# Kernel tuning notes

Hardware: AMD Instinct MI355X
Metric: run time of the kernel (lower is better)

Reference implementation:

```python
import jax, jax.numpy as jnp
import numpy as np

B, S, E, H, V, C = 1024, 64, 256, 512, 128, 32


def setup_inputs() -> dict:
    key = jax.random.key(0)
    ks = jax.random.split(key, 12)
    s = 0.05
    emb_table = jax.random.normal(ks[0], (V, E), jnp.float32) * s
    emb_table = emb_table.at[0].set(0.0)  # padding_idx = 0
    return {
        "x_in": jax.random.randint(ks[1], (B, S), 0, V),
        "x_lens": jax.random.randint(ks[2], (B,), 1, S + 1),
        "emb_table": emb_table,
        "W_ih": jax.random.normal(ks[3], (H, E), jnp.float32) * s,
        "b_ih": jnp.zeros((H,), jnp.float32),
        "W_hh": jax.random.normal(ks[4], (H, H), jnp.float32) * s,
        "b_hh": jnp.zeros((H,), jnp.float32),
        "W1": jax.random.normal(ks[5], (H, H), jnp.float32) * s,
        "b1": jnp.zeros((H,), jnp.float32),
        "W2": jax.random.normal(ks[6], (C, H), jnp.float32) * s,
        "b2": jnp.zeros((C,), jnp.float32),
    }


def reference(x_in, x_lens, emb_table, W_ih, b_ih, W_hh, b_hh, W1, b1, W2, b2):
    # Embedding lookup: [B, S, E]
    x_emb = emb_table[x_in]

    # Elman RNN: h_t = tanh(x_t W_ih^T + b_ih + h_{t-1} W_hh^T + b_hh)
    def step(h, x_t):
        h = jnp.tanh(x_t @ W_ih.T + b_ih + h @ W_hh.T + b_hh)
        return h, h

    h0 = jnp.zeros((x_in.shape[0], W_hh.shape[0]), x_emb.dtype)
    _, ys = jax.lax.scan(step, h0, jnp.swapaxes(x_emb, 0, 1))  # ys: [S, B, H]
    y_out = jnp.swapaxes(ys, 0, 1)  # [B, S, H]

    # column_gather: pick hidden state at position x_lens-1 for each row
    last = y_out[jnp.arange(y_out.shape[0]), x_lens - 1]  # [B, H]

    # MLP head (dropout is identity in eval mode)
    hidden = jax.nn.relu(last @ W1.T + b1)
    logits = hidden @ W2.T + b2  # [B, C]
    return logits
```

## Files before the change

kernel.cpp:

```cpp
#include <hip/hip_runtime.h>
#include <hip/hip_bf16.h>

#define BB 1024
#define SS 64
#define EE 256
#define HH 512
#define VV 128
#define CC 32

typedef _Float16 f16;
typedef _Float16 f16x4 __attribute__((ext_vector_type(4)));
typedef _Float16 f16x8 __attribute__((ext_vector_type(8)));
typedef float    f32x4 __attribute__((ext_vector_type(4)));

__global__ __launch_bounds__(256) void prep_P(
    const float* __restrict__ emb, const float* __restrict__ W_ih,
    const float* __restrict__ b_ih, const float* __restrict__ b_hh,
    f16* __restrict__ P)
{
    __shared__ float er[EE];
    const int v = blockIdx.x;
    for (int i = threadIdx.x; i < EE; i += 256) er[i] = emb[(size_t)v * EE + i];
    __syncthreads();
    for (int h = threadIdx.x; h < HH; h += 256) {
        const float4* wr = (const float4*)(W_ih + (size_t)h * EE);
        float s = 0.f;
        #pragma unroll 4
        for (int e4 = 0; e4 < EE / 4; ++e4) {
            float4 w = wr[e4];
            const float* e = er + e4 * 4;
            s += w.x * e[0] + w.y * e[1] + w.z * e[2] + w.w * e[3];
        }
        P[(size_t)v * HH + h] = (f16)(s + b_ih[h] + b_hh[h]);
    }
}

__global__ __launch_bounds__(256) void prep_W(
    const float* __restrict__ W_hh, f16* __restrict__ Wf)
{
    const int i = blockIdx.x * 256 + threadIdx.x;
    float4 x = ((const float4*)W_hh)[i];
    f16x4 y;
    y[0] = (f16)x.x; y[1] = (f16)x.y; y[2] = (f16)x.z; y[3] = (f16)x.w;
    *(f16x4*)(Wf + (size_t)i * 4) = y;
}

#define KSREG 12
#define KSLDS 4
#define HSTR  520

#define KB(t,k) "v"(bfr[t][k])
#define KBT(t)  KB(t,0), KB(t,1), KB(t,2), KB(t,3), KB(t,4), KB(t,5), \
                KB(t,6), KB(t,7), KB(t,8), KB(t,9), KB(t,10), KB(t,11)

__global__
__attribute__((amdgpu_flat_work_group_size(512, 512)))
__attribute__((amdgpu_waves_per_eu(2, 2)))
void rnn_kernel(
    const int* __restrict__ x_in, const int* __restrict__ x_lens,
    const f16* __restrict__ Wf, const f16* __restrict__ P,
    f16* __restrict__ last)
{
    __shared__ __align__(16) f16 hbuf[16 * HSTR];
    __shared__ __align__(16) f16 wlds[8 * 4 * KSLDS * 64 * 8];
    __shared__ int xin[16 * SS];
    __shared__ int lens[16];

    const int tid  = threadIdx.x;
    const int r0   = blockIdx.x * 16;
    const int wave = tid >> 6;
    const int lane = tid & 63;
    const int lrow = lane & 15;
    const int quad = lane >> 4;
    const int n0w  = wave * 64;

    f16x8 bfr[4][KSREG];
    #pragma unroll
    for (int t = 0; t < 4; ++t) {
        const f16* wr = Wf + (size_t)(n0w + 16 * t + lrow) * HH + quad * 8;
        #pragma unroll
        for (int ks = 0; ks < KSREG; ++ks)
            bfr[t][ks] = *(const f16x8*)(wr + ks * 32);
        #pragma unroll
        for (int ks = 0; ks < KSLDS; ++ks)
            *(f16x8*)(wlds + ((((wave * 4 + t) * KSLDS + ks) * 64 + lane) << 3)) =
                *(const f16x8*)(wr + (KSREG + ks) * 32);
    }

    for (int i = tid; i < 16 * (SS / 4); i += 512)
        ((int4*)xin)[i] = ((const int4*)(x_in + (size_t)r0 * SS))[i];
    if (tid < 16) lens[tid] = x_lens[r0 + tid];
    __syncthreads();

    const int   mylen = lens[lrow];
    const f16*  arow  = hbuf + lrow * HSTR + quad * 8;
    f16*        hwr   = hbuf + lrow * HSTR + n0w + quad * 4;
    f16*        lwr   = last + (size_t)(r0 + lrow) * HH + n0w + quad * 4;
    const f16*  pbase = P + n0w + quad * 4;

    for (int st = 0; st < SS; ++st) {
        asm volatile("" :: KBT(0), KBT(1), KBT(2), KBT(3));

        f32x4 acc0 = {0,0,0,0}, acc1 = {0,0,0,0}, acc2 = {0,0,0,0}, acc3 = {0,0,0,0};
        if (st) {
            #pragma unroll
            for (int ks = 0; ks < KSREG; ++ks) {
                f16x8 a = *(const f16x8*)(arow + ks * 32);
                acc0 = __builtin_amdgcn_mfma_f32_16x16x32_f16(bfr[0][ks], a, acc0, 0, 0, 0);
                acc1 = __builtin_amdgcn_mfma_f32_16x16x32_f16(bfr[1][ks], a, acc1, 0, 0, 0);
                acc2 = __builtin_amdgcn_mfma_f32_16x16x32_f16(bfr[2][ks], a, acc2, 0, 0, 0);
                acc3 = __builtin_amdgcn_mfma_f32_16x16x32_f16(bfr[3][ks], a, acc3, 0, 0, 0);
            }
            #pragma unroll
            for (int ks = 0; ks < KSLDS; ++ks) {
                f16x8 a  = *(const f16x8*)(arow + (KSREG + ks) * 32);
                f16x8 b0 = *(const f16x8*)(wlds + ((((wave * 4 + 0) * KSLDS + ks) * 64 + lane) << 3));
                f16x8 b1 = *(const f16x8*)(wlds + ((((wave * 4 + 1) * KSLDS + ks) * 64 + lane) << 3));
                f16x8 b2 = *(const f16x8*)(wlds + ((((wave * 4 + 2) * KSLDS + ks) * 64 + lane) << 3));
                f16x8 b3 = *(const f16x8*)(wlds + ((((wave * 4 + 3) * KSLDS + ks) * 64 + lane) << 3));
                acc0 = __builtin_amdgcn_mfma_f32_16x16x32_f16(b0, a, acc0, 0, 0, 0);
                acc1 = __builtin_amdgcn_mfma_f32_16x16x32_f16(b1, a, acc1, 0, 0, 0);
                acc2 = __builtin_amdgcn_mfma_f32_16x16x32_f16(b2, a, acc2, 0, 0, 0);
                acc3 = __builtin_amdgcn_mfma_f32_16x16x32_f16(b3, a, acc3, 0, 0, 0);
            }
        }

        const int  tok = xin[lrow * SS + st];
        const f16* pb  = pbase + (size_t)tok * HH;
        f16x4 pv0 = *(const f16x4*)(pb);
        f16x4 pv1 = *(const f16x4*)(pb + 16);
        f16x4 pv2 = *(const f16x4*)(pb + 32);
        f16x4 pv3 = *(const f16x4*)(pb + 48);

        __syncthreads();

        const int tp1 = st + 1;
        const bool wr_last = (mylen == tp1);
        #pragma unroll
        for (int t = 0; t < 4; ++t) {
            const f32x4 acc = (t == 0) ? acc0 : (t == 1) ? acc1 : (t == 2) ? acc2 : acc3;
            const f16x4 pv  = (t == 0) ? pv0  : (t == 1) ? pv1  : (t == 2) ? pv2  : pv3;
            f16x4 hv;
            #pragma unroll
            for (int r = 0; r < 4; ++r) {
                float z = acc[r] + (float)pv[r];
                float e = __expf(2.f * z);
                hv[r] = (f16)(1.f - 2.f / (e + 1.f));
            }
            *(f16x4*)(hwr + 16 * t) = hv;
            if (wr_last) *(f16x4*)(lwr + 16 * t) = hv;
        }

        __syncthreads();
    }
}

__global__ __launch_bounds__(256, 1)
void mlp1_kernel(
    const f16* __restrict__ last, const float* __restrict__ W1,
    const float* __restrict__ b1, f16* __restrict__ hidden)
{
    __shared__ __align__(16) f16 hb[16 * HSTR];
    const int tid   = threadIdx.x;
    const int g     = blockIdx.x & 63;
    const int slice = blockIdx.x >> 6;
    const int r0    = g * 16;
    const int n0    = slice * 64;
    const int wave  = tid >> 6;
    const int lane  = tid & 63;
    const int lrow  = lane & 15;
    const int quad  = lane >> 4;

    f16x8 bfr[16];
    {
        const float* wr = W1 + (size_t)(n0 + wave * 16 + lrow) * HH + quad * 8;
        #pragma unroll
        for (int K0 = 0; K0 < 16; ++K0) {
            float4 x0 = *(const float4*)(wr + K0 * 32);
            float4 x1 = *(const float4*)(wr + K0 * 32 + 4);
            f16x8 b;
            b[0] = (f16)x0.x; b[1] = (f16)x0.y; b[2] = (f16)x0.z; b[3] = (f16)x0.w;
            b[4] = (f16)x1.x; b[5] = (f16)x1.y; b[6] = (f16)x1.z; b[7] = (f16)x1.w;
            bfr[K0] = b;
        }
    }

    for (int i = tid; i < 16 * (HH / 8); i += 256) {
        const int row = i >> 6;
        const int c8  = (i & 63) * 8;
        *(float4*)(hb + row * HSTR + c8) =
            *(const float4*)(last + (size_t)(r0 + row) * HH + c8);
    }
    __syncthreads();

    f32x4 acc = {0,0,0,0};
    const f16* arow = hb + lrow * HSTR + quad * 8;
    #pragma unroll
    for (int K0 = 0; K0 < 16; ++K0) {
        f16x8 a = *(const f16x8*)(arow + K0 * 32);
        acc = __builtin_amdgcn_mfma_f32_16x16x32_f16(a, bfr[K0], acc, 0, 0, 0);
    }
    {
        const int cloc = wave * 16 + lrow;
        const float bb = b1[n0 + cloc];
        #pragma unroll
        for (int r = 0; r < 4; ++r) {
            const int row = quad * 4 + r;
            hidden[(size_t)(r0 + row) * HH + n0 + cloc] =
                (f16)fmaxf(acc[r] + bb, 0.f);
        }
    }
}

__global__ __launch_bounds__(256) void mlp2_kernel(
    const f16* __restrict__ hidden, const float* __restrict__ W2,
    const float* __restrict__ b2, float* __restrict__ out)
{
    __shared__ float hs[8][512];
    const int b0 = blockIdx.x * 8;
    for (int i = threadIdx.x; i < 8 * 512; i += 256)
        hs[i >> 9][i & 511] = (float)hidden[(size_t)(b0 + (i >> 9)) * HH + (i & 511)];
    __syncthreads();
    const int r = threadIdx.x >> 5, c = threadIdx.x & 31;
    const float4* w = (const float4*)(W2 + (size_t)c * HH);
    float acc = 0.f;
    #pragma unroll 4
    for (int k4 = 0; k4 < 128; ++k4) {
        float4 wv = w[k4];
        float4 hv = *(const float4*)(&hs[r][k4 * 4]);
        acc += wv.x * hv.x + wv.y * hv.y + wv.z * hv.z + wv.w * hv.w;
    }
    out[(size_t)(b0 + r) * CC + c] = acc + b2[c];
}

extern "C" void kernel_launch(void* const* d_in, const int* in_sizes, int n_in,
                              void* d_out, int out_size, void* d_ws, size_t ws_size,
                              hipStream_t stream)
{
    const int*   x_in   = (const int*)d_in[0];
    const int*   x_lens = (const int*)d_in[1];
    const float* emb    = (const float*)d_in[2];
    const float* W_ih   = (const float*)d_in[3];
    const float* b_ih   = (const float*)d_in[4];
    const float* W_hh   = (const float*)d_in[5];
    const float* b_hh   = (const float*)d_in[6];
    const float* W1     = (const float*)d_in[7];
    const float* b1     = (const float*)d_in[8];
    const float* W2     = (const float*)d_in[9];
    const float* b2     = (const float*)d_in[10];
    float* out = (float*)d_out;

    char* ws = (char*)d_ws;
    f16* P      = (f16*)ws;
    f16* last   = (f16*)(ws + (256 << 10));
    f16* hidden = (f16*)(ws + (256 << 10) + (1 << 20));
    f16* Wf     = hidden;

    hipLaunchKernelGGL(prep_P, dim3(VV), dim3(256), 0, stream,
                       emb, W_ih, b_ih, b_hh, P);
    hipLaunchKernelGGL(prep_W, dim3(256), dim3(256), 0, stream,
                       W_hh, Wf);
    hipLaunchKernelGGL(rnn_kernel, dim3(BB / 16), dim3(512), 0, stream,
                       x_in, x_lens, Wf, P, last);
    hipLaunchKernelGGL(mlp1_kernel, dim3(512), dim3(256), 0, stream,
                       last, W1, b1, hidden);
    hipLaunchKernelGGL(mlp2_kernel, dim3(BB / 8), dim3(256), 0, stream,
                       hidden, W2, b2, out);
}
```

Baseline: 299.5 us.

## Fuse MLP head into RNN kernel and merge prep kernels

```diff
diff --git a/kernel.cpp b/kernel.cpp
--- a/kernel.cpp
+++ b/kernel.cpp
@@ -13,36 +13,46 @@
 typedef _Float16 f16x8 __attribute__((ext_vector_type(8)));
 typedef float    f32x4 __attribute__((ext_vector_type(4)));
 
-__global__ __launch_bounds__(256) void prep_P(
+#define CVT_TOT4   (65536 + 65536 + 4096)
+#define CVT_STRIDE (96 * 256)
+
+__global__ __launch_bounds__(256) void prep_kernel(
     const float* __restrict__ emb, const float* __restrict__ W_ih,
     const float* __restrict__ b_ih, const float* __restrict__ b_hh,
-    f16* __restrict__ P)
+    const float* __restrict__ W_hh, const float* __restrict__ W1,
+    const float* __restrict__ W2,
+    f16* __restrict__ P, f16* __restrict__ Whf,
+    f16* __restrict__ W1f, f16* __restrict__ W2f)
 {
-    __shared__ float er[EE];
-    const int v = blockIdx.x;
-    for (int i = threadIdx.x; i < EE; i += 256) er[i] = emb[(size_t)v * EE + i];
-    __syncthreads();
-    for (int h = threadIdx.x; h < HH; h += 256) {
-        const float4* wr = (const float4*)(W_ih + (size_t)h * EE);
-        float s = 0.f;
-        #pragma unroll 4
-        for (int e4 = 0; e4 < EE / 4; ++e4) {
-            float4 w = wr[e4];
-            const float* e = er + e4 * 4;
-            s += w.x * e[0] + w.y * e[1] + w.z * e[2] + w.w * e[3];
-        }
-        P[(size_t)v * HH + h] = (f16)(s + b_ih[h] + b_hh[h]);
-    }
-}
-
-__global__ __launch_bounds__(256) void prep_W(
-    const float* __restrict__ W_hh, f16* __restrict__ Wf)
-{
-    const int i = blockIdx.x * 256 + threadIdx.x;
-    float4 x = ((const float4*)W_hh)[i];
-    f16x4 y;
-    y[0] = (f16)x.x; y[1] = (f16)x.y; y[2] = (f16)x.z; y[3] = (f16)x.w;
-    *(f16x4*)(Wf + (size_t)i * 4) = y;
+    if (blockIdx.x < VV) {
+        __shared__ float er[EE];
+        const int v = blockIdx.x;
+        for (int i = threadIdx.x; i < EE; i += 256) er[i] = emb[(size_t)v * EE + i];
+        __syncthreads();
+        for (int h = threadIdx.x; h < HH; h += 256) {
+            const float4* wr = (const float4*)(W_ih + (size_t)h * EE);
+            float s = 0.f;
+            #pragma unroll 4
+            for (int e4 = 0; e4 < EE / 4; ++e4) {
+                float4 w = wr[e4];
+                const float* e = er + e4 * 4;
+                s += w.x * e[0] + w.y * e[1] + w.z * e[2] + w.w * e[3];
+            }
+            P[(size_t)v * HH + h] = (f16)(s + b_ih[h] + b_hh[h]);
+        }
+    } else {
+        for (int i = (blockIdx.x - VV) * 256 + threadIdx.x; i < CVT_TOT4;
+             i += CVT_STRIDE) {
+            const float* src; f16* dst; int j;
+            if (i < 65536)       { src = W_hh; dst = Whf; j = i; }
+            else if (i < 131072) { src = W1;   dst = W1f; j = i - 65536; }
+            else                 { src = W2;   dst = W2f; j = i - 131072; }
+            float4 x = ((const float4*)src)[j];
+            f16x4 y;
+            y[0] = (f16)x.x; y[1] = (f16)x.y; y[2] = (f16)x.z; y[3] = (f16)x.w;
+            *(f16x4*)(dst + (size_t)j * 4) = y;
+        }
+    }
 }
 
 #define KSREG 12
@@ -56,10 +66,12 @@
 __global__
 __attribute__((amdgpu_flat_work_group_size(512, 512)))
 __attribute__((amdgpu_waves_per_eu(2, 2)))
-void rnn_kernel(
+void rnn_fused(
     const int* __restrict__ x_in, const int* __restrict__ x_lens,
-    const f16* __restrict__ Wf, const f16* __restrict__ P,
-    f16* __restrict__ last)
+    const f16* __restrict__ Whf, const f16* __restrict__ P,
+    const f16* __restrict__ W1f, const float* __restrict__ b1,
+    const f16* __restrict__ W2f, const float* __restrict__ b2,
+    float* __restrict__ out)
 {
     __shared__ __align__(16) f16 hbuf[16 * HSTR];
     __shared__ __align__(16) f16 wlds[8 * 4 * KSLDS * 64 * 8];
@@ -77,7 +89,7 @@
     f16x8 bfr[4][KSREG];
     #pragma unroll
     for (int t = 0; t < 4; ++t) {
-        const f16* wr = Wf + (size_t)(n0w + 16 * t + lrow) * HH + quad * 8;
+        const f16* wr = Whf + (size_t)(n0w + 16 * t + lrow) * HH + quad * 8;
         #pragma unroll
         for (int ks = 0; ks < KSREG; ++ks)
             bfr[t][ks] = *(const f16x8*)(wr + ks * 32);
@@ -95,8 +107,9 @@
     const int   mylen = lens[lrow];
     const f16*  arow  = hbuf + lrow * HSTR + quad * 8;
     f16*        hwr   = hbuf + lrow * HSTR + n0w + quad * 4;
-    f16*        lwr   = last + (size_t)(r0 + lrow) * HH + n0w + quad * 4;
     const f16*  pbase = P + n0w + quad * 4;
+
+    f16x4 lastreg[4];
 
     for (int st = 0; st < SS; ++st) {
         asm volatile("" :: KBT(0), KBT(1), KBT(2), KBT(3));
@@ -148,89 +161,65 @@
                 hv[r] = (f16)(1.f - 2.f / (e + 1.f));
             }
             *(f16x4*)(hwr + 16 * t) = hv;
-            if (wr_last) *(f16x4*)(lwr + 16 * t) = hv;
-        }
-
-        __syncthreads();
-    }
-}
-
-__global__ __launch_bounds__(256, 1)
-void mlp1_kernel(
-    const f16* __restrict__ last, const float* __restrict__ W1,
-    const float* __restrict__ b1, f16* __restrict__ hidden)
-{
-    __shared__ __align__(16) f16 hb[16 * HSTR];
-    const int tid   = threadIdx.x;
-    const int g     = blockIdx.x & 63;
-    const int slice = blockIdx.x >> 6;
-    const int r0    = g * 16;
-    const int n0    = slice * 64;
-    const int wave  = tid >> 6;
-    const int lane  = tid & 63;
-    const int lrow  = lane & 15;
-    const int quad  = lane >> 4;
-
-    f16x8 bfr[16];
+            if (wr_last) lastreg[t] = hv;
+        }
+
+        __syncthreads();
+    }
+
+    #pragma unroll
+    for (int t = 0; t < 4; ++t)
+        *(f16x4*)(hwr + 16 * t) = lastreg[t];
+    __syncthreads();
+
+    f16* hid = wlds;
     {
-        const float* wr = W1 + (size_t)(n0 + wave * 16 + lrow) * HH + quad * 8;
-        #pragma unroll
-        for (int K0 = 0; K0 < 16; ++K0) {
-            float4 x0 = *(const float4*)(wr + K0 * 32);
-            float4 x1 = *(const float4*)(wr + K0 * 32 + 4);
-            f16x8 b;
-            b[0] = (f16)x0.x; b[1] = (f16)x0.y; b[2] = (f16)x0.z; b[3] = (f16)x0.w;
-            b[4] = (f16)x1.x; b[5] = (f16)x1.y; b[6] = (f16)x1.z; b[7] = (f16)x1.w;
-            bfr[K0] = b;
-        }
-    }
-
-    for (int i = tid; i < 16 * (HH / 8); i += 256) {
-        const int row = i >> 6;
-        const int c8  = (i & 63) * 8;
-        *(float4*)(hb + row * HSTR + c8) =
-            *(const float4*)(last + (size_t)(r0 + row) * HH + c8);
+        f32x4 acc0 = {0,0,0,0}, acc1 = {0,0,0,0}, acc2 = {0,0,0,0}, acc3 = {0,0,0,0};
+        #pragma unroll 4
+        for (int ks = 0; ks < 16; ++ks) {
+            f16x8 a  = *(const f16x8*)(arow + ks * 32);
+            const f16* w1r = W1f + (size_t)(n0w + lrow) * HH + ks * 32 + quad * 8;
+            f16x8 b0 = *(const f16x8*)(w1r);
+            f16x8 b1 = *(const f16x8*)(w1r + 16 * HH);
+            f16x8 b2 = *(const f16x8*)(w1r + 32 * HH);
+            f16x8 b3 = *(const f16x8*)(w1r + 48 * HH);
+            acc0 = __builtin_amdgcn_mfma_f32_16x16x32_f16(b0, a, acc0, 0, 0, 0);
+            acc1 = __builtin_amdgcn_mfma_f32_16x16x32_f16(b1, a, acc1, 0, 0, 0);
+            acc2 = __builtin_amdgcn_mfma_f32_16x16x32_f16(b2, a, acc2, 0, 0, 0);
+            acc3 = __builtin_amdgcn_mfma_f32_16x16x32_f16(b3, a, acc3, 0, 0, 0);
+        }
+        __syncthreads();
+        f16* hwr2 = hid + lrow * HSTR + n0w + quad * 4;
+        #pragma unroll
+        for (int t = 0; t < 4; ++t) {
+            const f32x4 acc = (t == 0) ? acc0 : (t == 1) ? acc1 : (t == 2) ? acc2 : acc3;
+            const float4 bv = *(const float4*)(b1 + n0w + 16 * t + quad * 4);
+            const float  bb[4] = {bv.x, bv.y, bv.z, bv.w};
+            f16x4 hv;
+            #pragma unroll
+            for (int r = 0; r < 4; ++r)
+                hv[r] = (f16)fmaxf(acc[r] + bb[r], 0.f);
+            *(f16x4*)(hwr2 + 16 * t) = hv;
+        }
     }
     __syncthreads();
 
-    f32x4 acc = {0,0,0,0};
-    const f16* arow = hb + lrow * HSTR + quad * 8;
-    #pragma unroll
-    for (int K0 = 0; K0 < 16; ++K0) {
-        f16x8 a = *(const f16x8*)(arow + K0 * 32);
-        acc = __builtin_amdgcn_mfma_f32_16x16x32_f16(a, bfr[K0], acc, 0, 0, 0);
-    }
-    {
-        const int cloc = wave * 16 + lrow;
-        const float bb = b1[n0 + cloc];
-        #pragma unroll
-        for (int r = 0; r < 4; ++r) {
-            const int row = quad * 4 + r;
-            hidden[(size_t)(r0 + row) * HH + n0 + cloc] =
-                (f16)fmaxf(acc[r] + bb, 0.f);
-        }
-    }
-}
-
-__global__ __launch_bounds__(256) void mlp2_kernel(
-    const f16* __restrict__ hidden, const float* __restrict__ W2,
-    const float* __restrict__ b2, float* __restrict__ out)
-{
-    __shared__ float hs[8][512];
-    const int b0 = blockIdx.x * 8;
-    for (int i = threadIdx.x; i < 8 * 512; i += 256)
-        hs[i >> 9][i & 511] = (float)hidden[(size_t)(b0 + (i >> 9)) * HH + (i & 511)];
-    __syncthreads();
-    const int r = threadIdx.x >> 5, c = threadIdx.x & 31;
-    const float4* w = (const float4*)(W2 + (size_t)c * HH);
-    float acc = 0.f;
-    #pragma unroll 4
-    for (int k4 = 0; k4 < 128; ++k4) {
-        float4 wv = w[k4];
-        float4 hv = *(const float4*)(&hs[r][k4 * 4]);
-        acc += wv.x * hv.x + wv.y * hv.y + wv.z * hv.z + wv.w * hv.w;
-    }
-    out[(size_t)(b0 + r) * CC + c] = acc + b2[c];
+    if (wave < 2) {
+        const f16* harow = hid + lrow * HSTR + quad * 8;
+        f32x4 acc = {0,0,0,0};
+        #pragma unroll 4
+        for (int ks = 0; ks < 16; ++ks) {
+            f16x8 a = *(const f16x8*)(harow + ks * 32);
+            f16x8 b = *(const f16x8*)(W2f + (size_t)(wave * 16 + lrow) * HH
+                                      + ks * 32 + quad * 8);
+            acc = __builtin_amdgcn_mfma_f32_16x16x32_f16(b, a, acc, 0, 0, 0);
+        }
+        const float4 bv = *(const float4*)(b2 + wave * 16 + quad * 4);
+        float4 o;
+        o.x = acc[0] + bv.x; o.y = acc[1] + bv.y;
+        o.z = acc[2] + bv.z; o.w = acc[3] + bv.w;
+        *(float4*)(out + (size_t)(r0 + lrow) * CC + wave * 16 + quad * 4) = o;
+    }
 }
 
 extern "C" void kernel_launch(void* const* d_in, const int* in_sizes, int n_in,
@@ -251,19 +240,13 @@
     float* out = (float*)d_out;
 
     char* ws = (char*)d_ws;
-    f16* P      = (f16*)ws;
-    f16* last   = (f16*)(ws + (256 << 10));
-    f16* hidden = (f16*)(ws + (256 << 10) + (1 << 20));
-    f16* Wf     = hidden;
-
-    hipLaunchKernelGGL(prep_P, dim3(VV), dim3(256), 0, stream,
-                       emb, W_ih, b_ih, b_hh, P);
-    hipLaunchKernelGGL(prep_W, dim3(256), dim3(256), 0, stream,
-                       W_hh, Wf);
-    hipLaunchKernelGGL(rnn_kernel, dim3(BB / 16), dim3(512), 0, stream,
-                       x_in, x_lens, Wf, P, last);
-    hipLaunchKernelGGL(mlp1_kernel, dim3(512), dim3(256), 0, stream,
-                       last, W1, b1, hidden);
-    hipLaunchKernelGGL(mlp2_kernel, dim3(BB / 8), dim3(256), 0, stream,
-                       hidden, W2, b2, out);
+    f16* P   = (f16*)ws;
+    f16* Whf = (f16*)(ws + (256 << 10));
+    f16* W1f = (f16*)(ws + (256 << 10) + (512 << 10));
+    f16* W2f = (f16*)(ws + (256 << 10) + (1 << 20));
+
+    hipLaunchKernelGGL(prep_kernel, dim3(VV + 96), dim3(256), 0, stream,
+                       emb, W_ih, b_ih, b_hh, W_hh, W1, W2, P, Whf, W1f, W2f);
+    hipLaunchKernelGGL(rnn_fused, dim3(BB / 16), dim3(512), 0, stream,
+                       x_in, x_lens, Whf, P, W1f, b1, W2f, b2, out);
 }
```

Result: faster. 278.0 us (-7.2%).
